# Kernel optimization log

Measured on AMD Instinct MI355X. Metric: run time of the kernel, lower is better.

Reference implementation:

```python
import jax, jax.numpy as jnp
import numpy as np

NEG_INF = -jnp.inf


def setup_inputs() -> dict:
    B, V = 128, 128000
    key = jax.random.key(0)
    k1, k2, k3, k4, k5 = jax.random.split(key, 5)
    logits = jax.random.normal(k1, (B, V), dtype=jnp.float32)
    # temperatures in [0.1, 1.0) to avoid divide-by-tiny blowups
    temperatures = jax.random.uniform(k2, (B,), dtype=jnp.float32) * 0.9 + 0.1
    # min_p typically small, in [0, 0.1)
    min_ps = jax.random.uniform(k3, (B,), dtype=jnp.float32) * 0.1
    # top_p in [0.1, 1.0)
    top_ps = jax.random.uniform(k4, (B,), dtype=jnp.float32) * 0.9 + 0.1
    # top_k in [1, 1000)
    top_ks = jax.random.randint(k5, (B,), 1, 1000, dtype=jnp.int32)
    return {"logits": logits, "temperatures": temperatures, "min_ps": min_ps,
            "top_ps": top_ps, "top_ks": top_ks}


def _apply_top_k_top_p(logits, top_ps, top_ks):
    B, V = logits.shape
    sort_idx = jnp.argsort(logits, axis=-1)  # ascending, matches torch sort(descending=False)
    logits_sort = jnp.take_along_axis(logits, sort_idx, axis=-1)
    # top-k: threshold is the (V-k)-th smallest value; mask anything strictly below it
    thresh_idx = (V - top_ks.astype(jnp.int32))[:, None]          # [B,1]
    thresh = jnp.take_along_axis(logits_sort, thresh_idx, axis=-1)  # [B,1]
    logits_sort = jnp.where(logits_sort < thresh, NEG_INF, logits_sort)
    # top-p: drop smallest tokens whose cumulative prob <= 1 - p; never drop the max token
    probs_sort = jax.nn.softmax(logits_sort, axis=-1)
    probs_sum = jnp.cumsum(probs_sort, axis=-1)
    top_p_mask = probs_sum <= (1.0 - top_ps)[:, None]
    top_p_mask = top_p_mask.at[:, -1].set(False)
    logits_sort = jnp.where(top_p_mask, NEG_INF, logits_sort)
    # scatter back to original vocab order
    rows = jnp.arange(B)[:, None]
    return jnp.zeros_like(logits_sort).at[rows, sort_idx].set(logits_sort)


def _apply_min_p(logits, min_ps):
    probs = jax.nn.softmax(logits, axis=-1)
    top_probs = jnp.max(probs, axis=-1, keepdims=True)
    remove = probs < min_ps[:, None] * top_probs
    return jnp.where(remove, NEG_INF, logits)


def reference(logits, temperatures, min_ps, top_ps, top_ks):
    logits = logits.astype(jnp.float32) / temperatures[:, None]
    logits = _apply_top_k_top_p(logits, top_ps, top_ks)
    logits = _apply_min_p(logits, min_ps)
    # torch.multinomial(softmax(logits), 1) == categorical sampling from logits
    sample_key = jax.random.key(42)
    next_tokens = jax.random.categorical(sample_key, logits, axis=-1)  # [B]
    return next_tokens
```

## Files before the change

### kernel.cpp

```cpp
#include <hip/hip_runtime.h>
#include <stdint.h>

#define HBINS 4096
#define CAND 2048
#define NSLICES 16
#define HTHREADS 256
#define CTHREADS 256
#define STHREADS 1024

typedef unsigned int u32;
typedef unsigned long long u64;

__device__ __forceinline__ u32 f2s(float f) {
  u32 b = __float_as_uint(f);
  return b ^ ((b & 0x80000000u) ? 0xFFFFFFFFu : 0x80000000u);
}
__device__ __forceinline__ float s2f(u32 s) {
  u32 b = (s & 0x80000000u) ? (s ^ 0x80000000u) : ~s;
  return __uint_as_float(b);
}
__device__ __forceinline__ u32 rotl32(u32 x, int r) { return (x << r) | (x >> (32 - r)); }

__device__ __forceinline__ u64 shfl_xor_u64(u64 v, int mask) {
  int lo = __shfl_xor((int)(u32)v, mask, 64);
  int hi = __shfl_xor((int)(u32)(v >> 32), mask, 64);
  return ((u64)(u32)hi << 32) | (u32)lo;
}

__device__ __forceinline__ u32 threefry_bits(u32 ctr) {
  const u32 ks0 = 0u, ks1 = 42u, ks2 = 0x1BD11BDAu ^ 0u ^ 42u;
  u32 x0 = ks0;
  u32 x1 = ctr + ks1;
#define TFR(r) { x0 += x1; x1 = rotl32(x1, (r)); x1 ^= x0; }
  TFR(13) TFR(15) TFR(26) TFR(6)   x0 += ks1; x1 += ks2 + 1u;
  TFR(17) TFR(29) TFR(16) TFR(24)  x0 += ks2; x1 += ks0 + 2u;
  TFR(13) TFR(15) TFR(26) TFR(6)   x0 += ks0; x1 += ks1 + 3u;
  TFR(17) TFR(29) TFR(16) TFR(24)  x0 += ks1; x1 += ks2 + 4u;
  TFR(13) TFR(15) TFR(26) TFR(6)   x0 += ks2; x1 += ks0 + 5u;
#undef TFR
  return x0 ^ x1;
}

__global__ __launch_bounds__(1024)
void zero_kernel(u32* __restrict__ p, int n) {
  int i = blockIdx.x * 1024 + threadIdx.x;
  if (i < n) p[i] = 0u;
}

__global__ __launch_bounds__(HTHREADS)
void hist_kernel(const float* __restrict__ logits, u32* __restrict__ ghist,
                 int V, int slice_len) {
  const int row = blockIdx.x / NSLICES;
  const int sl  = blockIdx.x % NSLICES;
  const int tid = threadIdx.x;
  __shared__ u32 h[HBINS];
  for (int i = tid; i < HBINS; i += HTHREADS) h[i] = 0u;
  __syncthreads();
  int rem = V - sl * slice_len;
  if (rem > slice_len) rem = slice_len;
  if (rem < 0) rem = 0;
  const float* src = logits + (size_t)row * (size_t)V + (size_t)sl * slice_len;
  const int n4 = rem >> 2;
  const float4* p4 = (const float4*)src;
  for (int i = tid; i < n4; i += HTHREADS) {
    float4 w = p4[i];
    atomicAdd(&h[f2s(w.x) >> 20], 1u);
    atomicAdd(&h[f2s(w.y) >> 20], 1u);
    atomicAdd(&h[f2s(w.z) >> 20], 1u);
    atomicAdd(&h[f2s(w.w) >> 20], 1u);
  }
  for (int i = (n4 << 2) + tid; i < rem; i += HTHREADS)
    atomicAdd(&h[f2s(src[i]) >> 20], 1u);
  __syncthreads();
  u32* gh = ghist + (size_t)row * HBINS;
  for (int i = tid; i < HBINS; i += HTHREADS) {
    u32 c = h[i];
    if (c) atomicAdd(&gh[i], c);
  }
}

__global__ __launch_bounds__(256)
void select_kernel(const u32* __restrict__ ghist, const int* __restrict__ topks,
                   u32* __restrict__ gthr, u32* __restrict__ gcs,
                   u32* __restrict__ gcount, int V) {
  const int row = blockIdx.x;
  const int tid = threadIdx.x;
  __shared__ u32 hist[HBINS];
  __shared__ u32 part[256];
  __shared__ u32 chunk[64];
  const u32* gh = ghist + (size_t)row * HBINS;
  for (int i = tid; i < HBINS; i += 256) hist[i] = gh[i];
  __syncthreads();
  {
    u32 s = 0;
    for (int j = 0; j < 16; ++j) s += hist[tid * 16 + j];
    part[tid] = s;
  }
  __syncthreads();
  if (tid < 64) {
    chunk[tid] = part[tid * 4] + part[tid * 4 + 1] + part[tid * 4 + 2] + part[tid * 4 + 3];
  }
  __syncthreads();
  if (tid == 0) {
    int k = topks[row];
    if (k < 1) k = 1;
    if (k > V) k = V;
    const u32 ku = (u32)k;
    u32 acc = 0;
    int cstar = 0;
    for (int c = 63; c >= 0; --c) {
      if (acc + chunk[c] >= ku) { cstar = c; break; }
      acc += chunk[c];
    }
    int pstar = cstar * 4;
    for (int p = cstar * 4 + 3; p >= cstar * 4; --p) {
      if (acc + part[p] >= ku) { pstar = p; break; }
      acc += part[p];
    }
    int bstar = pstar * 16;
    for (int bq = pstar * 16 + 15; bq >= pstar * 16; --bq) {
      acc += hist[bq];
      if (acc >= ku) { bstar = bq; break; }
    }
    gthr[row] = (u32)bstar << 20;
    gcs[row] = (acc < (u32)CAND ? acc : (u32)CAND);
    gcount[row] = 0u;
  }
}

__global__ __launch_bounds__(CTHREADS)
void collect_kernel(const float* __restrict__ logits,
                    const float* __restrict__ temps,
                    const u32* __restrict__ gthr,
                    u32* __restrict__ gcount,
                    u64* __restrict__ gcand, int V, int slice_len) {
  const int row = blockIdx.x / NSLICES;
  const int sl  = blockIdx.x % NSLICES;
  const int tid = threadIdx.x;

  __shared__ u64 stage[CAND];
  __shared__ int sh_cnt, sh_base;
  if (tid == 0) sh_cnt = 0;
  __syncthreads();

  const u32 thr = gthr[row];
  const float t = temps[row];
  int rem = V - sl * slice_len;
  if (rem > slice_len) rem = slice_len;
  if (rem < 0) rem = 0;
  const float* src = logits + (size_t)row * (size_t)V + (size_t)sl * slice_len;
  const u32 ibase = (u32)(sl * slice_len);
  const int n4 = rem >> 2;
  const float4* p4 = (const float4*)src;
  for (int i = tid; i < n4; i += CTHREADS) {
    float4 w = p4[i];
    if (f2s(w.x) >= thr) { int pos = atomicAdd(&sh_cnt, 1); if (pos < CAND) stage[pos] = ((u64)f2s(w.x / t) << 32) | (ibase + 4u * i + 0u); }
    if (f2s(w.y) >= thr) { int pos = atomicAdd(&sh_cnt, 1); if (pos < CAND) stage[pos] = ((u64)f2s(w.y / t) << 32) | (ibase + 4u * i + 1u); }
    if (f2s(w.z) >= thr) { int pos = atomicAdd(&sh_cnt, 1); if (pos < CAND) stage[pos] = ((u64)f2s(w.z / t) << 32) | (ibase + 4u * i + 2u); }
    if (f2s(w.w) >= thr) { int pos = atomicAdd(&sh_cnt, 1); if (pos < CAND) stage[pos] = ((u64)f2s(w.w / t) << 32) | (ibase + 4u * i + 3u); }
  }
  for (int i = (n4 << 2) + tid; i < rem; i += CTHREADS) {
    float l = src[i];
    if (f2s(l) >= thr) { int pos = atomicAdd(&sh_cnt, 1); if (pos < CAND) stage[pos] = ((u64)f2s(l / t) << 32) | (ibase + (u32)i); }
  }
  __syncthreads();
  int n = sh_cnt;
  if (n > CAND) n = CAND;
  if (tid == 0) sh_base = (int)atomicAdd(&gcount[row], (u32)n);
  __syncthreads();
  const int base = sh_base;
  u64* gc = gcand + (size_t)row * CAND;
  for (int i = tid; i < n; i += CTHREADS) {
    int dst = base + i;
    if (dst < CAND) gc[dst] = stage[i];
  }
}

__global__ __launch_bounds__(STHREADS)
void Sampler_73529840107542_kernel(const float* __restrict__ minps,
                                   const float* __restrict__ topps,
                                   const int* __restrict__ topks,
                                   const u32* __restrict__ gcs,
                                   const u64* __restrict__ gcand,
                                   int* __restrict__ out, int V) {
  const int b = blockIdx.x;
  const int tid = threadIdx.x;
  const int w = tid >> 6;
  const int l = tid & 63;
  const float one_minus_p = 1.0f - topps[b];
  const float minp = minps[b];
  int k = topks[b];
  if (k < 1) k = 1;
  if (k > V) k = V;

  __shared__ __align__(16) unsigned char arena[34816];
  u64* cand   = (u64*)(arena);
  float* bufA = (float*)(arena + 16384);
  float* bufB = (float*)(arena + 24576);
  unsigned char* keepf = arena + 32768;
  u64* red64  = (u64*)(arena + 16384);
  float* redA = (float*)(arena + 16384);
  float* redB = (float*)(arena + 24576);

  __shared__ int sh_lb;
  __shared__ u32 sh_Ts;
  __shared__ float sh_m, sh_Z1, sh_Z2;

  const int cs = (int)gcs[b];
  const u64* gc = gcand + (size_t)b * CAND;
  const int e_lo = (w << 7) + l;
  const int e_hi = e_lo + 64;
  const u64 SENT = 0xFFFFFFFFFFFFFFFFull;
  u64 k0 = (e_lo < cs) ? gc[e_lo] : SENT;
  u64 k1 = (e_hi < cs) ? gc[e_hi] : SENT;

  for (int size = 2; size <= CAND; size <<= 1) {
    for (int s = size >> 1; s > 0; s >>= 1) {
      if (s >= 128) {
        cand[e_lo] = k0; cand[e_hi] = k1;
        __syncthreads();
        u64 p0 = cand[e_lo ^ s], p1 = cand[e_hi ^ s];
        {
          bool keepmin = (((e_lo & s) == 0) == ((e_lo & size) == 0));
          if (keepmin ? (p0 < k0) : (p0 > k0)) k0 = p0;
        }
        {
          bool keepmin = (((e_hi & s) == 0) == ((e_hi & size) == 0));
          if (keepmin ? (p1 < k1) : (p1 > k1)) k1 = p1;
        }
        __syncthreads();
      } else if (s == 64) {
        bool asc = ((e_lo & size) == 0);
        if ((k0 > k1) == asc) { u64 t = k0; k0 = k1; k1 = t; }
      } else {
        u64 p0 = shfl_xor_u64(k0, s);
        u64 p1 = shfl_xor_u64(k1, s);
        {
          bool keepmin = (((l & s) == 0) == ((e_lo & size) == 0));
          if (keepmin ? (p0 < k0) : (p0 > k0)) k0 = p0;
        }
        {
          bool keepmin = (((l & s) == 0) == ((e_hi & size) == 0));
          if (keepmin ? (p1 < k1) : (p1 > k1)) k1 = p1;
        }
      }
    }
  }
  cand[e_lo] = k0; cand[e_hi] = k1;
  __syncthreads();

  if (tid == 0) {
    int ti = cs - k; if (ti < 0) ti = 0;
    sh_Ts = (u32)(cand[ti] >> 32);
    sh_m  = s2f((u32)(cand[cs - 1] >> 32));
  }
  __syncthreads();
  const u32 Ts = sh_Ts;
  const float m = sh_m;

  for (int c = tid; c < cs; c += STHREADS) {
    u32 s = (u32)(cand[c] >> 32);
    if (s >= Ts && (c == 0 || (u32)(cand[c - 1] >> 32) < Ts)) sh_lb = c;
  }
  __syncthreads();
  const int lb = sh_lb;

  for (int c = tid; c < CAND; c += STHREADS) {
    float e = 0.0f;
    if (c < cs) {
      u32 s = (u32)(cand[c] >> 32);
      if (s >= Ts) e = expf(s2f(s) - m);
    }
    bufA[c] = e;
  }
  __syncthreads();

  {
    float local = bufA[tid] + bufA[tid + STHREADS];
    redB[tid] = local;
    __syncthreads();
    for (int s = STHREADS >> 1; s > 0; s >>= 1) {
      if (tid < s) redB[tid] += redB[tid + s];
      __syncthreads();
    }
    if (tid == 0) sh_Z1 = redB[0];
    __syncthreads();
  }

  const float Z1 = sh_Z1;
  for (int c = tid; c < CAND; c += STHREADS) bufA[c] = bufA[c] / Z1;
  __syncthreads();

  if (w == 0) {
    float carry = 0.0f;
    for (int base = lb; base < cs; base += 64) {
      int c = base + l;
      float v = (c < cs) ? bufA[c] : 0.0f;
      float acc = carry;
      for (int j = 0; j < 64; ++j) {
        float t = __shfl(v, j, 64);
        acc += (l >= j) ? t : 0.0f;
      }
      if (c < cs) bufB[c] = acc;
      carry = __shfl(acc, 63, 64);
    }
  }
  __syncthreads();

  for (int c = tid; c < CAND; c += STHREADS) {
    unsigned char kf = 0;
    if (c < cs) {
      u32 s = (u32)(cand[c] >> 32);
      if (s >= Ts && (c == cs - 1 || bufB[c] > one_minus_p)) kf = 1;
    }
    keepf[c] = kf;
  }
  __syncthreads();

  {
    float local = 0.0f;
    for (int c = tid; c < CAND; c += STHREADS) {
      if (keepf[c]) {
        u32 s = (u32)(cand[c] >> 32);
        local += expf(s2f(s) - m);
      }
    }
    redA[tid] = local;
    __syncthreads();
    for (int s = STHREADS >> 1; s > 0; s >>= 1) {
      if (tid < s) redA[tid] += redA[tid + s];
      __syncthreads();
    }
    if (tid == 0) sh_Z2 = redA[0];
    __syncthreads();
  }

  {
    const float Z2 = sh_Z2;
    const float rhs = minp * (1.0f / Z2);
    for (int c = tid; c < CAND; c += STHREADS) {
      if (keepf[c]) {
        u32 s = (u32)(cand[c] >> 32);
        float p2 = expf(s2f(s) - m) / Z2;
        if (p2 < rhs) keepf[c] = 0;
      }
    }
  }
  __syncthreads();

  {
    const float TINY = 1.17549435082228750797e-38f;
    u64 best = 0ull;
    for (int c = lb + tid; c < cs; c += STHREADS) {
      if (!keepf[c]) continue;
      u32 s = (u32)(cand[c] >> 32);
      u32 idx = (u32)(cand[c] & 0xFFFFFFFFull);
      float x = s2f(s);
      u32 bits = threefry_bits((u32)b * (u32)V + idx);
      float f = __uint_as_float((bits >> 9) | 0x3f800000u) - 1.0f;
      float u = fmaxf(TINY, f * 1.0f + TINY);
      float g = -logf(-logf(u));
      float sc = g + x;
      u64 key = ((u64)f2s(sc) << 32) | (u64)(0xFFFFFFFFu - idx);
      if (key > best) best = key;
    }
    red64[tid] = best;
    __syncthreads();
    for (int s = STHREADS >> 1; s > 0; s >>= 1) {
      if (tid < s) { u64 o = red64[tid + s]; if (o > red64[tid]) red64[tid] = o; }
      __syncthreads();
    }
    if (tid == 0) out[b] = (int)(0xFFFFFFFFu - (u32)(red64[0] & 0xFFFFFFFFull));
  }
}

extern "C" void kernel_launch(void* const* d_in, const int* in_sizes, int n_in,
                              void* d_out, int out_size, void* d_ws, size_t ws_size,
                              hipStream_t stream) {
  const float* logits = (const float*)d_in[0];
  const float* temps  = (const float*)d_in[1];
  const float* minps  = (const float*)d_in[2];
  const float* topps  = (const float*)d_in[3];
  const int*   topks  = (const int*)d_in[4];
  const int B = in_sizes[1];
  const int V = in_sizes[0] / B;
  (void)n_in; (void)out_size; (void)ws_size;

  u32* ghist  = (u32*)d_ws;
  u32* gcount = ghist + (size_t)B * HBINS;
  u32* gcs    = gcount + B;
  u32* gthr   = gcs + B;
  u64* gcand  = (u64*)(gthr + B);

  const int nz = B * HBINS;
  const int slice_len = (((V + NSLICES - 1) / NSLICES) + 3) & ~3;

  zero_kernel<<<dim3((nz + 1023) / 1024), dim3(1024), 0, stream>>>(ghist, nz);
  hist_kernel<<<dim3(B * NSLICES), dim3(HTHREADS), 0, stream>>>(logits, ghist, V, slice_len);
  select_kernel<<<dim3(B), dim3(256), 0, stream>>>(ghist, topks, gthr, gcs, gcount, V);
  collect_kernel<<<dim3(B * NSLICES), dim3(CTHREADS), 0, stream>>>(
      logits, temps, gthr, gcount, gcand, V, slice_len);
  Sampler_73529840107542_kernel<<<dim3(B), dim3(STHREADS), 0, stream>>>(
      minps, topps, topks, gcs, gcand, (int*)d_out, V);
}
```

Baseline: 170.5 us.

## Radix-select top-k threshold and sort only surviving candidates in sampler

```diff
diff --git a/kernel.cpp b/kernel.cpp
--- a/kernel.cpp
+++ b/kernel.cpp
@@ -3,7 +3,7 @@
 
 #define HBINS 4096
 #define CAND 2048
-#define NSLICES 16
+#define NSLICES 32
 #define HTHREADS 256
 #define CTHREADS 256
 #define STHREADS 1024
@@ -41,12 +41,6 @@
   return x0 ^ x1;
 }
 
-__global__ __launch_bounds__(1024)
-void zero_kernel(u32* __restrict__ p, int n) {
-  int i = blockIdx.x * 1024 + threadIdx.x;
-  if (i < n) p[i] = 0u;
-}
-
 __global__ __launch_bounds__(HTHREADS)
 void hist_kernel(const float* __restrict__ logits, u32* __restrict__ ghist,
                  int V, int slice_len) {
@@ -97,9 +91,8 @@
     part[tid] = s;
   }
   __syncthreads();
-  if (tid < 64) {
+  if (tid < 64)
     chunk[tid] = part[tid * 4] + part[tid * 4 + 1] + part[tid * 4 + 2] + part[tid * 4 + 3];
-  }
   __syncthreads();
   if (tid == 0) {
     int k = topks[row];
@@ -185,176 +178,202 @@
                                    int* __restrict__ out, int V) {
   const int b = blockIdx.x;
   const int tid = threadIdx.x;
-  const int w = tid >> 6;
-  const int l = tid & 63;
+  const int w = tid >> 6, l = tid & 63;
   const float one_minus_p = 1.0f - topps[b];
   const float minp = minps[b];
   int k = topks[b];
   if (k < 1) k = 1;
   if (k > V) k = V;
 
-  __shared__ __align__(16) unsigned char arena[34816];
-  u64* cand   = (u64*)(arena);
-  float* bufA = (float*)(arena + 16384);
-  float* bufB = (float*)(arena + 24576);
-  unsigned char* keepf = arena + 32768;
-  u64* red64  = (u64*)(arena + 16384);
-  float* redA = (float*)(arena + 16384);
-  float* redB = (float*)(arena + 24576);
-
-  __shared__ int sh_lb;
-  __shared__ u32 sh_Ts;
-  __shared__ float sh_m, sh_Z1, sh_Z2;
+  __shared__ u64 cand[CAND];
+  __shared__ u64 scand[CAND];
+  __shared__ float eBuf[CAND];
+  __shared__ float bufA[CAND];
+  __shared__ float bufB[CAND];
+  __shared__ unsigned char keepf[CAND];
+  __shared__ u32 rbin[256];
+  __shared__ float wredf[16];
+  __shared__ u64 wred64[16];
+  __shared__ int sh_byte, sh_above, sh_ns;
+  __shared__ float sh_Z1, sh_Z2;
 
   const int cs = (int)gcs[b];
   const u64* gc = gcand + (size_t)b * CAND;
+  for (int c = tid; c < cs; c += STHREADS) cand[c] = gc[c];
+  if (tid == 0) sh_ns = 0;
+  __syncthreads();
+
+  u32 prefix = 0u;
+  u32 remk = (u32)k;
+  for (int pass = 0; pass < 4; ++pass) {
+    const int shift = 24 - 8 * pass;
+    if (tid < 256) rbin[tid] = 0u;
+    __syncthreads();
+    const u32 mask = (pass == 0) ? 0u : (0xFFFFFFFFu << (shift + 8));
+    for (int c = tid; c < cs; c += STHREADS) {
+      u32 s = (u32)(cand[c] >> 32);
+      if (((s ^ prefix) & mask) == 0u)
+        atomicAdd(&rbin[(s >> shift) & 255u], 1u);
+    }
+    __syncthreads();
+    if (w == 0) {
+      u32 b0 = rbin[4 * l], b1 = rbin[4 * l + 1], b2 = rbin[4 * l + 2], b3 = rbin[4 * l + 3];
+      u32 q3 = b3, q2 = b2 + q3, q1 = b1 + q2, q0 = b0 + q1;
+      u32 inc = q0;
+      #pragma unroll
+      for (int off = 1; off < 64; off <<= 1) {
+        int src = l + off;
+        u32 o = (u32)__shfl((int)inc, src < 64 ? src : l, 64);
+        inc += (src < 64) ? o : 0u;
+      }
+      u32 excl = inc - q0;
+      u64 ball = __ballot(excl + q0 >= remk);
+      int lsel = 63 - __clzll(ball);
+      if (l == lsel) {
+        int i; u32 above;
+        if      (excl + q3 >= remk) { i = 3; above = excl; }
+        else if (excl + q2 >= remk) { i = 2; above = excl + q3; }
+        else if (excl + q1 >= remk) { i = 1; above = excl + q2; }
+        else                        { i = 0; above = excl + q1; }
+        sh_byte = 4 * l + i;
+        sh_above = (int)above;
+      }
+    }
+    __syncthreads();
+    prefix |= ((u32)sh_byte) << shift;
+    remk -= (u32)sh_above;
+  }
+  const u32 Ts = prefix;
+
+  for (int c = tid; c < cs; c += STHREADS) {
+    u64 key = cand[c];
+    if ((u32)(key >> 32) >= Ts) {
+      int pos = atomicAdd(&sh_ns, 1);
+      scand[pos] = key;
+    }
+  }
+  __syncthreads();
+  const int ns = sh_ns;
+
+  int SN = 128;
+  while (SN < ns) SN <<= 1;
+  const int NW = SN >> 7;
+  const bool act = (w < NW);
   const int e_lo = (w << 7) + l;
   const int e_hi = e_lo + 64;
   const u64 SENT = 0xFFFFFFFFFFFFFFFFull;
-  u64 k0 = (e_lo < cs) ? gc[e_lo] : SENT;
-  u64 k1 = (e_hi < cs) ? gc[e_hi] : SENT;
-
-  for (int size = 2; size <= CAND; size <<= 1) {
+  u64 k0 = (act && e_lo < ns) ? scand[e_lo] : SENT;
+  u64 k1 = (act && e_hi < ns) ? scand[e_hi] : SENT;
+  for (int size = 2; size <= SN; size <<= 1) {
     for (int s = size >> 1; s > 0; s >>= 1) {
       if (s >= 128) {
-        cand[e_lo] = k0; cand[e_hi] = k1;
+        if (act) { scand[e_lo] = k0; scand[e_hi] = k1; }
         __syncthreads();
-        u64 p0 = cand[e_lo ^ s], p1 = cand[e_hi ^ s];
-        {
-          bool keepmin = (((e_lo & s) == 0) == ((e_lo & size) == 0));
-          if (keepmin ? (p0 < k0) : (p0 > k0)) k0 = p0;
-        }
-        {
-          bool keepmin = (((e_hi & s) == 0) == ((e_hi & size) == 0));
-          if (keepmin ? (p1 < k1) : (p1 > k1)) k1 = p1;
+        if (act) {
+          u64 p0 = scand[e_lo ^ s], p1 = scand[e_hi ^ s];
+          bool km0 = (((e_lo & s) == 0) == ((e_lo & size) == 0));
+          if (km0 ? (p0 < k0) : (p0 > k0)) k0 = p0;
+          bool km1 = (((e_hi & s) == 0) == ((e_hi & size) == 0));
+          if (km1 ? (p1 < k1) : (p1 > k1)) k1 = p1;
         }
         __syncthreads();
-      } else if (s == 64) {
-        bool asc = ((e_lo & size) == 0);
-        if ((k0 > k1) == asc) { u64 t = k0; k0 = k1; k1 = t; }
-      } else {
-        u64 p0 = shfl_xor_u64(k0, s);
-        u64 p1 = shfl_xor_u64(k1, s);
-        {
-          bool keepmin = (((l & s) == 0) == ((e_lo & size) == 0));
-          if (keepmin ? (p0 < k0) : (p0 > k0)) k0 = p0;
-        }
-        {
-          bool keepmin = (((l & s) == 0) == ((e_hi & size) == 0));
-          if (keepmin ? (p1 < k1) : (p1 > k1)) k1 = p1;
+      } else if (act) {
+        if (s == 64) {
+          bool asc = ((e_lo & size) == 0);
+          if ((k0 > k1) == asc) { u64 t = k0; k0 = k1; k1 = t; }
+        } else {
+          u64 p0 = shfl_xor_u64(k0, s);
+          u64 p1 = shfl_xor_u64(k1, s);
+          bool km0 = (((l & s) == 0) == ((e_lo & size) == 0));
+          if (km0 ? (p0 < k0) : (p0 > k0)) k0 = p0;
+          bool km1 = (((l & s) == 0) == ((e_hi & size) == 0));
+          if (km1 ? (p1 < k1) : (p1 > k1)) k1 = p1;
         }
       }
     }
   }
-  cand[e_lo] = k0; cand[e_hi] = k1;
-  __syncthreads();
-
-  if (tid == 0) {
-    int ti = cs - k; if (ti < 0) ti = 0;
-    sh_Ts = (u32)(cand[ti] >> 32);
-    sh_m  = s2f((u32)(cand[cs - 1] >> 32));
-  }
-  __syncthreads();
-  const u32 Ts = sh_Ts;
-  const float m = sh_m;
-
-  for (int c = tid; c < cs; c += STHREADS) {
-    u32 s = (u32)(cand[c] >> 32);
-    if (s >= Ts && (c == 0 || (u32)(cand[c - 1] >> 32) < Ts)) sh_lb = c;
-  }
-  __syncthreads();
-  const int lb = sh_lb;
-
-  for (int c = tid; c < CAND; c += STHREADS) {
-    float e = 0.0f;
-    if (c < cs) {
-      u32 s = (u32)(cand[c] >> 32);
-      if (s >= Ts) e = expf(s2f(s) - m);
-    }
-    bufA[c] = e;
-  }
+  if (act) { scand[e_lo] = k0; scand[e_hi] = k1; }
+  __syncthreads();
+
+  const float m = s2f((u32)(scand[ns - 1] >> 32));
+
+  for (int c = tid; c < ns; c += STHREADS)
+    eBuf[c] = expf(s2f((u32)(scand[c] >> 32)) - m);
   __syncthreads();
 
   {
-    float local = bufA[tid] + bufA[tid + STHREADS];
-    redB[tid] = local;
-    __syncthreads();
-    for (int s = STHREADS >> 1; s > 0; s >>= 1) {
-      if (tid < s) redB[tid] += redB[tid + s];
-      __syncthreads();
-    }
-    if (tid == 0) sh_Z1 = redB[0];
+    float local = 0.0f;
+    for (int c = tid; c < ns; c += STHREADS) local += eBuf[c];
+    #pragma unroll
+    for (int off = 1; off < 64; off <<= 1) local += __shfl_xor(local, off, 64);
+    if (l == 0) wredf[w] = local;
+    __syncthreads();
+    if (w == 0) {
+      float v = (l < 16) ? wredf[l] : 0.0f;
+      #pragma unroll
+      for (int off = 1; off < 64; off <<= 1) v += __shfl_xor(v, off, 64);
+      if (l == 0) sh_Z1 = v;
+    }
     __syncthreads();
   }
 
   const float Z1 = sh_Z1;
-  for (int c = tid; c < CAND; c += STHREADS) bufA[c] = bufA[c] / Z1;
+  for (int c = tid; c < ns; c += STHREADS) bufA[c] = eBuf[c] / Z1;
   __syncthreads();
 
   if (w == 0) {
     float carry = 0.0f;
-    for (int base = lb; base < cs; base += 64) {
+    for (int base = 0; base < ns; base += 64) {
       int c = base + l;
-      float v = (c < cs) ? bufA[c] : 0.0f;
+      float v = (c < ns) ? bufA[c] : 0.0f;
       float acc = carry;
+      #pragma unroll 16
       for (int j = 0; j < 64; ++j) {
         float t = __shfl(v, j, 64);
         acc += (l >= j) ? t : 0.0f;
       }
-      if (c < cs) bufB[c] = acc;
+      if (c < ns) bufB[c] = acc;
       carry = __shfl(acc, 63, 64);
     }
   }
   __syncthreads();
 
-  for (int c = tid; c < CAND; c += STHREADS) {
-    unsigned char kf = 0;
-    if (c < cs) {
-      u32 s = (u32)(cand[c] >> 32);
-      if (s >= Ts && (c == cs - 1 || bufB[c] > one_minus_p)) kf = 1;
-    }
-    keepf[c] = kf;
-  }
+  for (int c = tid; c < ns; c += STHREADS)
+    keepf[c] = (c == ns - 1 || bufB[c] > one_minus_p) ? 1 : 0;
   __syncthreads();
 
   {
     float local = 0.0f;
-    for (int c = tid; c < CAND; c += STHREADS) {
-      if (keepf[c]) {
-        u32 s = (u32)(cand[c] >> 32);
-        local += expf(s2f(s) - m);
-      }
-    }
-    redA[tid] = local;
-    __syncthreads();
-    for (int s = STHREADS >> 1; s > 0; s >>= 1) {
-      if (tid < s) redA[tid] += redA[tid + s];
-      __syncthreads();
-    }
-    if (tid == 0) sh_Z2 = redA[0];
+    for (int c = tid; c < ns; c += STHREADS)
+      if (keepf[c]) local += eBuf[c];
+    #pragma unroll
+    for (int off = 1; off < 64; off <<= 1) local += __shfl_xor(local, off, 64);
+    if (l == 0) wredf[w] = local;
+    __syncthreads();
+    if (w == 0) {
+      float v = (l < 16) ? wredf[l] : 0.0f;
+      #pragma unroll
+      for (int off = 1; off < 64; off <<= 1) v += __shfl_xor(v, off, 64);
+      if (l == 0) sh_Z2 = v;
+    }
     __syncthreads();
   }
 
   {
     const float Z2 = sh_Z2;
     const float rhs = minp * (1.0f / Z2);
-    for (int c = tid; c < CAND; c += STHREADS) {
-      if (keepf[c]) {
-        u32 s = (u32)(cand[c] >> 32);
-        float p2 = expf(s2f(s) - m) / Z2;
-        if (p2 < rhs) keepf[c] = 0;
-      }
-    }
+    for (int c = tid; c < ns; c += STHREADS)
+      if (keepf[c] && (eBuf[c] / Z2 < rhs)) keepf[c] = 0;
   }
   __syncthreads();
 
   {
     const float TINY = 1.17549435082228750797e-38f;
     u64 best = 0ull;
-    for (int c = lb + tid; c < cs; c += STHREADS) {
+    for (int c = tid; c < ns; c += STHREADS) {
       if (!keepf[c]) continue;
-      u32 s = (u32)(cand[c] >> 32);
-      u32 idx = (u32)(cand[c] & 0xFFFFFFFFull);
+      u32 s = (u32)(scand[c] >> 32);
+      u32 idx = (u32)(scand[c] & 0xFFFFFFFFull);
       float x = s2f(s);
       u32 bits = threefry_bits((u32)b * (u32)V + idx);
       float f = __uint_as_float((bits >> 9) | 0x3f800000u) - 1.0f;
@@ -364,13 +383,22 @@
       u64 key = ((u64)f2s(sc) << 32) | (u64)(0xFFFFFFFFu - idx);
       if (key > best) best = key;
     }
-    red64[tid] = best;
-    __syncthreads();
-    for (int s = STHREADS >> 1; s > 0; s >>= 1) {
-      if (tid < s) { u64 o = red64[tid + s]; if (o > red64[tid]) red64[tid] = o; }
-      __syncthreads();
-    }
-    if (tid == 0) out[b] = (int)(0xFFFFFFFFu - (u32)(red64[0] & 0xFFFFFFFFull));
+    #pragma unroll
+    for (int off = 1; off < 64; off <<= 1) {
+      u64 o = shfl_xor_u64(best, off);
+      if (o > best) best = o;
+    }
+    if (l == 0) wred64[w] = best;
+    __syncthreads();
+    if (w == 0) {
+      u64 v = (l < 16) ? wred64[l] : 0ull;
+      #pragma unroll
+      for (int off = 1; off < 64; off <<= 1) {
+        u64 o = shfl_xor_u64(v, off);
+        if (o > v) v = o;
+      }
+      if (l == 0) out[b] = (int)(0xFFFFFFFFu - (u32)(v & 0xFFFFFFFFull));
+    }
   }
 }
 
@@ -392,10 +420,9 @@
   u32* gthr   = gcs + B;
   u64* gcand  = (u64*)(gthr + B);
 
-  const int nz = B * HBINS;
   const int slice_len = (((V + NSLICES - 1) / NSLICES) + 3) & ~3;
 
-  zero_kernel<<<dim3((nz + 1023) / 1024), dim3(1024), 0, stream>>>(ghist, nz);
+  hipMemsetAsync(ghist, 0, (size_t)B * HBINS * sizeof(u32), stream);
   hist_kernel<<<dim3(B * NSLICES), dim3(HTHREADS), 0, stream>>>(logits, ghist, V, slice_len);
   select_kernel<<<dim3(B), dim3(256), 0, stream>>>(ghist, topks, gthr, gcs, gcount, V);
   collect_kernel<<<dim3(B * NSLICES), dim3(CTHREADS), 0, stream>>>(
```

After: 179.0 us. +5.0%, slower.
